# Performance work log

Measured on AMD Instinct MI355X. Metric: run time of the kernel, lower is better.

## Reference

```python
import jax, jax.numpy as jnp
import numpy as np

EPS = 1.1920929e-07  # torch fp32 RMSNorm default eps

def rmsnorm(x, w):
    return x * jax.lax.rsqrt(jnp.mean(x * x, axis=-1, keepdims=True) + EPS) * w

def causal_conv1d(x, w, b):
    # x: [B, L, di], w: [di, dc] depthwise kernel, b: [di]
    di, dc = w.shape
    xt = jnp.swapaxes(x, 1, 2)                       # [B, di, L]
    xt = jnp.pad(xt, ((0, 0), (0, 0), (dc - 1, 0)))  # causal left pad
    out = jax.lax.conv_general_dilated(
        xt, w[:, None, :], window_strides=(1,), padding='VALID',
        feature_group_count=di, dimension_numbers=('NCH', 'OIH', 'NCH'))
    return jnp.swapaxes(out + b[None, :, None], 1, 2)  # [B, L, di]

def selective_scan(u, dt, Bm, Cm, A, Dp):
    # u, dt: [B, L, di]; Bm, Cm: [B, L, ds]; A: [di, ds]; Dp: [di]
    Bsz, L, di = u.shape
    ds = A.shape[1]
    def step(h, inp):
        dt_t, B_t, C_t, u_t = inp
        dA = jnp.exp(dt_t[..., None] * A)                           # [B, di, ds]
        dBu = dt_t[..., None] * B_t[:, None, :] * u_t[..., None]    # [B, di, ds]
        h = dA * h + dBu
        y = jnp.einsum('bds,bs->bd', h, C_t)
        return h, y
    h0 = jnp.zeros((Bsz, di, ds), u.dtype)
    xs = (jnp.swapaxes(dt, 0, 1), jnp.swapaxes(Bm, 0, 1),
          jnp.swapaxes(Cm, 0, 1), jnp.swapaxes(u, 0, 1))
    _, ys = jax.lax.scan(step, h0, xs)                # ys: [L, B, di]
    return jnp.swapaxes(ys, 0, 1) + u * Dp            # skip connection D*u

def mamba_block(x, in_w, cw, cb, xp_w, dtp_w, dtp_b, a_log, dp, out_w, d_state, dt_rank):
    di = a_log.shape[0]
    xz = jnp.einsum('bld,ed->ble', x, in_w)           # [B, L, 2*di]
    x_in, z = xz[..., :di], xz[..., di:]
    xc = jax.nn.silu(causal_conv1d(x_in, cw, cb))     # [B, L, di]
    x_dbl = jnp.einsum('bld,ed->ble', xc, xp_w)       # [B, L, dt_rank+2*ds]
    dt = x_dbl[..., :dt_rank]
    Bm = x_dbl[..., dt_rank:dt_rank + d_state]
    Cm = x_dbl[..., dt_rank + d_state:]
    dt = jax.nn.softplus(jnp.einsum('blr,dr->bld', dt, dtp_w) + dtp_b)
    A = -jnp.exp(a_log)                               # [di, ds]
    y = selective_scan(xc, dt, Bm, Cm, A, dp)
    y = y * jax.nn.silu(z)
    return jnp.einsum('bld,ed->ble', y, out_w)        # [B, L, d_model]

def mlp(x, w1, b1, w2, b2):
    h = jax.nn.gelu(jnp.einsum('bld,ed->ble', x, w1) + b1, approximate=False)
    return jax.nn.gelu(jnp.einsum('ble,de->bld', h, w2) + b2, approximate=False)

def reference(x, in_proj_w, conv_w, conv_b, x_proj_w, dt_proj_w, dt_proj_b,
              A_log, D_param, out_proj_w, mlp_w1, mlp_b1, mlp_w2, mlp_b2,
              ln_w, ln2_w):
    d_state = A_log.shape[-1]
    dt_rank = dt_proj_w.shape[-1]
    num_layers = in_proj_w.shape[0]
    residual2 = x
    for i in range(num_layers):
        residual = x
        x = mamba_block(x, in_proj_w[i], conv_w[i], conv_b[i], x_proj_w[i],
                        dt_proj_w[i], dt_proj_b[i], A_log[i], D_param[i],
                        out_proj_w[i], d_state, dt_rank)
        x = mlp(x, mlp_w1, mlp_b1, mlp_w2, mlp_b2)
        x = rmsnorm(x + residual, ln_w)
    return rmsnorm(x + residual2, ln2_w)

def setup_inputs() -> dict:
    key = jax.random.key(0)
    ks = jax.random.split(key, 16)
    B, L, D = 4, 2048, 1024
    NL, di, ds, dc, dtr = 2, 2048, 16, 4, 64
    s = 0.02
    return {
        'x': jax.random.normal(ks[0], (B, L, D), jnp.float32),
        'in_proj_w': jax.random.normal(ks[1], (NL, 2 * di, D), jnp.float32) * s,
        'conv_w': jax.random.normal(ks[2], (NL, di, dc), jnp.float32) * 0.3,
        'conv_b': jax.random.normal(ks[3], (NL, di), jnp.float32) * 0.02,
        'x_proj_w': jax.random.normal(ks[4], (NL, dtr + 2 * ds, di), jnp.float32) * s,
        'dt_proj_w': jax.random.normal(ks[5], (NL, di, dtr), jnp.float32) * 0.1,
        'dt_proj_b': jax.random.normal(ks[6], (NL, di), jnp.float32) * 0.5 - 4.0,
        'A_log': jnp.log(jax.random.uniform(ks[7], (NL, di, ds), jnp.float32, 1.0, 16.0)),
        'D_param': jax.random.normal(ks[8], (NL, di), jnp.float32),
        'out_proj_w': jax.random.normal(ks[9], (NL, D, di), jnp.float32) * s,
        'mlp_w1': jax.random.normal(ks[10], (2 * D, D), jnp.float32) * s,
        'mlp_b1': jnp.zeros((2 * D,), jnp.float32),
        'mlp_w2': jax.random.normal(ks[11], (D, 2 * D), jnp.float32) * s,
        'mlp_b2': jnp.zeros((D,), jnp.float32),
        'ln_w': jnp.ones((D,), jnp.float32),
        'ln2_w': jnp.ones((D,), jnp.float32),
    }
```

## Files before the change

### kernel.cpp

```cpp
#include <hip/hip_runtime.h>
#include <math.h>

namespace {

constexpr int Bsz = 4;
constexpr int L   = 2048;
constexpr int D   = 1024;
constexpr int DI  = 2048;
constexpr int DSTATE = 16;
constexpr int DTR = 64;
constexpr int ML  = Bsz * L;
constexpr int NCH = 32;
constexpr int CL  = 64;

typedef __attribute__((ext_vector_type(8))) short bfrag;
typedef __attribute__((ext_vector_type(4))) float f32x4;

__device__ __forceinline__ unsigned short f2b(float f) {
  union { float f; unsigned int u; } c; c.f = f;
  unsigned int u = c.u;
  unsigned int r = (u + 0x7fffu + ((u >> 16) & 1u)) >> 16;
  return (unsigned short)r;
}
__device__ __forceinline__ float b2f(unsigned short h) {
  union { unsigned int u; float f; } c; c.u = ((unsigned int)h) << 16;
  return c.f;
}

__device__ __forceinline__ void async16(const void* g, void* l) {
  __builtin_amdgcn_global_load_lds(
      (const __attribute__((address_space(1))) void*)g,
      (__attribute__((address_space(3))) void*)l, 16, 0, 0);
}

template<int ACT>
__device__ __forceinline__ float activate(float x) {
  if (ACT == 1) { return x / (1.f + expf(-x)); }
  if (ACT == 2) { return 0.5f * x * (1.f + erff(x * 0.7071067811865475f)); }
  if (ACT == 3) { return (x > 20.f) ? x : log1pf(expf(x)); }
  return x;
}

template<int ACT, bool HAS_BIAS, int BN, bool SPLIT>
__global__ __launch_bounds__(512) void gemm2(
    const unsigned short* __restrict__ A, long lda,
    const unsigned short* __restrict__ W, long ldw,
    const float* __restrict__ bias,
    unsigned short* __restrict__ C0,
    unsigned short* __restrict__ C1,
    long ldc, int K)
{
  constexpr int NB   = BN / 64;
  constexpr int ABUF = 256 * 64;
  constexpr int BBUF = BN * 64;
  constexpr int NLA  = 4;
  constexpr int NLB  = NB;
  constexpr int NL   = NLA + NLB;
  __shared__ unsigned short lds[2 * ABUF + 2 * BBUF];

  const int tid  = threadIdx.x;
  const int lane = tid & 63;
  const int wid  = tid >> 6;
  const int wr   = wid >> 2;
  const int wc   = wid & 3;
  const int frow = lane & 15;
  const int klg  = lane >> 4;

  const int gx = gridDim.x;
  int id = blockIdx.y * gx + blockIdx.x;
  const int q = (gx * gridDim.y) >> 3;
  id = (id & 7) * q + (id >> 3);
  const int bx = id % gx;
  const int by = id / gx;
  const long bm = (long)by * 256;
  const long bn = (long)bx * BN;

  unsigned short* Cb;
  long cbase;
  if (SPLIT) {
    if (bn < 2048) { Cb = C0; cbase = bn; }
    else           { Cb = C1; cbase = bn - 2048; }
  } else { Cb = C0; cbase = bn; }

  f32x4 acc[8][NB];
  #pragma unroll
  for (int m = 0; m < 8; ++m)
    #pragma unroll
    for (int n = 0; n < NB; ++n)
      acc[m][n] = (f32x4){0.f, 0.f, 0.f, 0.f};

  auto stage = [&](int kt, int p) {
    const long kcol = (long)kt * 64;
    #pragma unroll
    for (int l = 0; l < NLA; ++l) {
      const int idx = tid + l * 512;
      const int row = idx >> 3;
      const int ch  = (idx & 7) ^ (row & 7);
      async16(A + (bm + row) * lda + kcol + ch * 8,
              &lds[p * ABUF + idx * 8]);
    }
    #pragma unroll
    for (int l = 0; l < NLB; ++l) {
      const int idx = tid + l * 512;
      const int row = idx >> 3;
      const int ch  = (idx & 7) ^ (row & 7);
      async16(W + (bn + row) * ldw + kcol + ch * 8,
              &lds[2 * ABUF + p * BBUF + idx * 8]);
    }
  };

  const int NT = K >> 6;
  stage(0, 0);
  stage(1, 1);
  asm volatile("s_waitcnt vmcnt(%0)" :: "n"(NL) : "memory");
  __builtin_amdgcn_sched_barrier(0);
  __builtin_amdgcn_s_barrier();

  for (int kt = 0; kt < NT; ++kt) {
    const unsigned short* Ab = &lds[(kt & 1) * ABUF];
    const unsigned short* Bb = &lds[2 * ABUF + (kt & 1) * BBUF];
    __builtin_amdgcn_s_setprio(1);
    #pragma unroll
    for (int kk = 0; kk < 2; ++kk) {
      bfrag av[8], bv[NB];
      #pragma unroll
      for (int m = 0; m < 8; ++m) {
        const int r  = wr * 128 + m * 16 + frow;
        const int ch = (kk * 4 + klg) ^ (r & 7);
        av[m] = *reinterpret_cast<const bfrag*>(&Ab[r * 64 + ch * 8]);
      }
      #pragma unroll
      for (int n = 0; n < NB; ++n) {
        const int r  = wc * (BN / 4) + n * 16 + frow;
        const int ch = (kk * 4 + klg) ^ (r & 7);
        bv[n] = *reinterpret_cast<const bfrag*>(&Bb[r * 64 + ch * 8]);
      }
      #pragma unroll
      for (int m = 0; m < 8; ++m)
        #pragma unroll
        for (int n = 0; n < NB; ++n)
          acc[m][n] = __builtin_amdgcn_mfma_f32_16x16x32_bf16(bv[n], av[m], acc[m][n], 0, 0, 0);
    }
    __builtin_amdgcn_s_setprio(0);
    if (kt + 1 == NT) break;
    __builtin_amdgcn_sched_barrier(0);
    __builtin_amdgcn_s_barrier();
    if (kt + 2 < NT) {
      stage(kt + 2, kt & 1);
      asm volatile("s_waitcnt vmcnt(%0)" :: "n"(NL) : "memory");
    } else {
      asm volatile("s_waitcnt vmcnt(0)" ::: "memory");
    }
    __builtin_amdgcn_sched_barrier(0);
    __builtin_amdgcn_s_barrier();
  }

  #pragma unroll
  for (int n = 0; n < NB; ++n) {
    const long coff = wc * (BN / 4) + n * 16 + klg * 4;
    float4 b4 = make_float4(0.f, 0.f, 0.f, 0.f);
    if (HAS_BIAS) b4 = *reinterpret_cast<const float4*>(&bias[bn + coff]);
    #pragma unroll
    for (int m = 0; m < 8; ++m) {
      const long row = bm + wr * 128 + m * 16 + frow;
      const float v0 = activate<ACT>(acc[m][n][0] + b4.x);
      const float v1 = activate<ACT>(acc[m][n][1] + b4.y);
      const float v2 = activate<ACT>(acc[m][n][2] + b4.z);
      const float v3 = activate<ACT>(acc[m][n][3] + b4.w);
      ushort4 o; o.x = f2b(v0); o.y = f2b(v1); o.z = f2b(v2); o.w = f2b(v3);
      *reinterpret_cast<ushort4*>(&Cb[row * ldc + cbase + coff]) = o;
    }
  }
}

template<int ACT, bool HAS_BIAS>
__global__ __launch_bounds__(256) void gemm_mfma(
    const unsigned short* __restrict__ A, long lda,
    const unsigned short* __restrict__ W, long ldw,
    const float* __restrict__ bias,
    unsigned short* __restrict__ C, long ldc,
    int K)
{
  __shared__ unsigned short As[128 * 32];
  __shared__ unsigned short Bs[128 * 32];
  const int tid  = threadIdx.x;
  const int lane = tid & 63;
  const int w    = tid >> 6;
  const int wr   = w >> 1, wc = w & 1;
  const long bm = (long)blockIdx.y * 128;
  const long bn = (long)blockIdx.x * 128;

  const int srow = tid >> 2;
  const int scol = (tid & 3) * 8;
  const unsigned short* ga0 = A + (bm + srow)      * lda + scol;
  const unsigned short* ga1 = A + (bm + 64 + srow) * lda + scol;
  const unsigned short* gb0 = W + (bn + srow)      * ldw + scol;
  const unsigned short* gb1 = W + (bn + 64 + srow) * ldw + scol;
  char* lA = (char*)As;
  char* lB = (char*)Bs;
  const int loff = tid * 16;

  const int frow = lane & 15;
  const int klg  = lane >> 4;
  const int fko  = klg * 8;

  f32x4 acc[4][4];
  #pragma unroll
  for (int m = 0; m < 4; ++m)
    #pragma unroll
    for (int n = 0; n < 4; ++n)
      acc[m][n] = (f32x4){0.f, 0.f, 0.f, 0.f};

  for (int k0 = 0; k0 < K; k0 += 32) {
    __syncthreads();
    async16(ga0 + k0, lA + loff);
    async16(ga1 + k0, lA + 4096 + loff);
    async16(gb0 + k0, lB + loff);
    async16(gb1 + k0, lB + 4096 + loff);
    __syncthreads();
    bfrag a[4], b[4];
    #pragma unroll
    for (int m = 0; m < 4; ++m)
      a[m] = *reinterpret_cast<const bfrag*>(&As[(wr*64 + m*16 + frow)*32 + fko]);
    #pragma unroll
    for (int n = 0; n < 4; ++n)
      b[n] = *reinterpret_cast<const bfrag*>(&Bs[(wc*64 + n*16 + frow)*32 + fko]);
    #pragma unroll
    for (int m = 0; m < 4; ++m)
      #pragma unroll
      for (int n = 0; n < 4; ++n)
        acc[m][n] = __builtin_amdgcn_mfma_f32_16x16x32_bf16(b[n], a[m], acc[m][n], 0, 0, 0);
  }

  #pragma unroll
  for (int n = 0; n < 4; ++n) {
    const long col = bn + wc*64 + n*16 + klg*4;
    float4 b4 = make_float4(0.f, 0.f, 0.f, 0.f);
    if (HAS_BIAS) b4 = *reinterpret_cast<const float4*>(&bias[col]);
    #pragma unroll
    for (int m = 0; m < 4; ++m) {
      const long row = bm + wr*64 + m*16 + frow;
      const float v0 = activate<ACT>(acc[m][n][0] + b4.x);
      const float v1 = activate<ACT>(acc[m][n][1] + b4.y);
      const float v2 = activate<ACT>(acc[m][n][2] + b4.z);
      const float v3 = activate<ACT>(acc[m][n][3] + b4.w);
      ushort4 o; o.x = f2b(v0); o.y = f2b(v1); o.z = f2b(v2); o.w = f2b(v3);
      *reinterpret_cast<ushort4*>(&C[row * ldc + col]) = o;
    }
  }
}

__global__ __launch_bounds__(256) void xproj_mfma(
    const unsigned short* __restrict__ A,
    const unsigned short* __restrict__ W,
    float* __restrict__ xdbl,
    unsigned short* __restrict__ dtr)
{
  constexpr int ABUF = 64 * 64;
  constexpr int BBUF = 96 * 64;
  constexpr int NL   = 5;
  __shared__ unsigned short lds[2 * ABUF + 2 * BBUF];

  const int tid  = threadIdx.x;
  const int lane = tid & 63;
  const int wv   = tid >> 6;
  const int frow = lane & 15;
  const int klg  = lane >> 4;
  const long bm  = (long)blockIdx.x * 64;

  f32x4 acc[6];
  #pragma unroll
  for (int n = 0; n < 6; ++n) acc[n] = (f32x4){0.f, 0.f, 0.f, 0.f};

  auto stage = [&](int kt, int p) {
    const long kcol = (long)kt * 64;
    #pragma unroll
    for (int l = 0; l < 2; ++l) {
      const int idx = tid + l * 256;
      const int row = idx >> 3;
      const int ch  = (idx & 7) ^ (row & 7);
      async16(A + (bm + row) * DI + kcol + ch * 8,
              &lds[p * ABUF + idx * 8]);
    }
    #pragma unroll
    for (int l = 0; l < 3; ++l) {
      const int idx = tid + l * 256;
      const int row = idx >> 3;
      const int ch  = (idx & 7) ^ (row & 7);
      async16(W + (long)row * DI + kcol + ch * 8,
              &lds[2 * ABUF + p * BBUF + idx * 8]);
    }
  };

  constexpr int NT = DI / 64;
  stage(0, 0);
  stage(1, 1);
  asm volatile("s_waitcnt vmcnt(%0)" :: "n"(NL) : "memory");
  __builtin_amdgcn_sched_barrier(0);
  __builtin_amdgcn_s_barrier();

  for (int kt = 0; kt < NT; ++kt) {
    const unsigned short* Ab = &lds[(kt & 1) * ABUF];
    const unsigned short* Bb = &lds[2 * ABUF + (kt & 1) * BBUF];
    __builtin_amdgcn_s_setprio(1);
    #pragma unroll
    for (int kk = 0; kk < 2; ++kk) {
      const int ra = wv * 16 + frow;
      const int cha = (kk * 4 + klg) ^ (ra & 7);
      const bfrag a = *reinterpret_cast<const bfrag*>(&Ab[ra * 64 + cha * 8]);
      #pragma unroll
      for (int n = 0; n < 6; ++n) {
        const int rb = n * 16 + frow;
        const int chb = (kk * 4 + klg) ^ (rb & 7);
        const bfrag b = *reinterpret_cast<const bfrag*>(&Bb[rb * 64 + chb * 8]);
        acc[n] = __builtin_amdgcn_mfma_f32_16x16x32_bf16(b, a, acc[n], 0, 0, 0);
      }
    }
    __builtin_amdgcn_s_setprio(0);
    if (kt + 1 == NT) break;
    __builtin_amdgcn_sched_barrier(0);
    __builtin_amdgcn_s_barrier();
    if (kt + 2 < NT) {
      stage(kt + 2, kt & 1);
      asm volatile("s_waitcnt vmcnt(%0)" :: "n"(NL) : "memory");
    } else {
      asm volatile("s_waitcnt vmcnt(0)" ::: "memory");
    }
    __builtin_amdgcn_sched_barrier(0);
    __builtin_amdgcn_s_barrier();
  }

  const long row = bm + wv*16 + frow;
  #pragma unroll
  for (int n = 0; n < 6; ++n) {
    const int col = n*16 + klg*4;
    float4 v; v.x = acc[n][0]; v.y = acc[n][1]; v.z = acc[n][2]; v.w = acc[n][3];
    *reinterpret_cast<float4*>(&xdbl[row * 96 + col]) = v;
    if (n < 4) {
      ushort4 o; o.x = f2b(v.x); o.y = f2b(v.y); o.z = f2b(v.z); o.w = f2b(v.w);
      *reinterpret_cast<ushort4*>(&dtr[row * 64 + col]) = o;
    }
  }
}

__global__ __launch_bounds__(256) void cvt_all(
    const float* __restrict__ s0, unsigned short* __restrict__ d0, long n0,
    const float* __restrict__ s1, unsigned short* __restrict__ d1, long n1,
    const float* __restrict__ s2, unsigned short* __restrict__ d2, long n2,
    const float* __restrict__ s3, unsigned short* __restrict__ d3, long n3,
    const float* __restrict__ s4, unsigned short* __restrict__ d4, long n4,
    const float* __restrict__ s5, unsigned short* __restrict__ d5, long n5,
    const float* __restrict__ s6, unsigned short* __restrict__ d6, long n6)
{
  long i = (long)blockIdx.x * 256 + threadIdx.x;
  const float* s; unsigned short* d;
  if      (i < n0)                    { s = s0; d = d0; }
  else if ((i -= n0) < n1)            { s = s1; d = d1; }
  else if ((i -= n1) < n2)            { s = s2; d = d2; }
  else if ((i -= n2) < n3)            { s = s3; d = d3; }
  else if ((i -= n3) < n4)            { s = s4; d = d4; }
  else if ((i -= n4) < n5)            { s = s5; d = d5; }
  else if ((i -= n5) < n6)            { s = s6; d = d6; }
  else return;
  const float4 v = reinterpret_cast<const float4*>(s)[i];
  ushort4 o; o.x = f2b(v.x); o.y = f2b(v.y); o.z = f2b(v.z); o.w = f2b(v.w);
  reinterpret_cast<ushort4*>(d)[i] = o;
}

__global__ __launch_bounds__(256) void conv_silu(
    const unsigned short* __restrict__ xin,
    const float* __restrict__ w,
    const float* __restrict__ bias,
    unsigned short* __restrict__ xc)
{
  const int idx = blockIdx.x * 256 + threadIdx.x;
  const int D4 = DI / 4;
  const int d  = (idx % D4) * 4;
  const int bt = idx / D4;
  const int t  = bt & (L - 1);
  const int b  = bt >> 11;
  const float4 w0 = *reinterpret_cast<const float4*>(w + (long)(d+0)*4);
  const float4 w1 = *reinterpret_cast<const float4*>(w + (long)(d+1)*4);
  const float4 w2 = *reinterpret_cast<const float4*>(w + (long)(d+2)*4);
  const float4 w3 = *reinterpret_cast<const float4*>(w + (long)(d+3)*4);
  const float4 bv = *reinterpret_cast<const float4*>(bias + d);
  float a0 = bv.x, a1 = bv.y, a2 = bv.z, a3 = bv.w;
  const float wk0[4] = {w0.x, w0.y, w0.z, w0.w};
  const float wk1[4] = {w1.x, w1.y, w1.z, w1.w};
  const float wk2[4] = {w2.x, w2.y, w2.z, w2.w};
  const float wk3[4] = {w3.x, w3.y, w3.z, w3.w};
  #pragma unroll
  for (int k = 0; k < 4; ++k) {
    const int tt = t - 3 + k;
    if (tt >= 0) {
      const ushort4 xv = *reinterpret_cast<const ushort4*>(xin + ((long)(b * L + tt)) * DI + d);
      a0 = fmaf(wk0[k], b2f(xv.x), a0);
      a1 = fmaf(wk1[k], b2f(xv.y), a1);
      a2 = fmaf(wk2[k], b2f(xv.z), a2);
      a3 = fmaf(wk3[k], b2f(xv.w), a3);
    }
  }
  a0 = a0 / (1.f + expf(-a0));
  a1 = a1 / (1.f + expf(-a1));
  a2 = a2 / (1.f + expf(-a2));
  a3 = a3 / (1.f + expf(-a3));
  ushort4 o; o.x = f2b(a0); o.y = f2b(a1); o.z = f2b(a2); o.w = f2b(a3);
  *reinterpret_cast<ushort4*>(xc + (long)bt * DI + d) = o;
}

__global__ __launch_bounds__(256) void scan_p1(
    const unsigned short* __restrict__ dt,
    const unsigned short* __restrict__ u,
    const float* __restrict__ xdbl,
    const float* __restrict__ a_log,
    float* __restrict__ hend,
    float* __restrict__ sdt)
{
  const int bid = blockIdx.x;
  const int dg = bid & 7;
  const int c  = (bid >> 3) & (NCH - 1);
  const int b  = bid >> 8;
  const int d  = dg * 256 + threadIdx.x;
  float A[16];
  #pragma unroll
  for (int q = 0; q < 4; ++q) {
    const float4 al = *reinterpret_cast<const float4*>(a_log + (long)d * 16 + q * 4);
    A[q*4+0] = -__expf(al.x); A[q*4+1] = -__expf(al.y);
    A[q*4+2] = -__expf(al.z); A[q*4+3] = -__expf(al.w);
  }
  float h[16];
  #pragma unroll
  for (int s = 0; s < 16; ++s) h[s] = 0.f;
  float s_dt = 0.f;
  const long row0 = (long)b * L + (long)c * CL;

  float dtv = b2f(dt[row0 * DI + d]);
  float uv  = b2f(u [row0 * DI + d]);
  float4 Bq[4];
  #pragma unroll
  for (int q = 0; q < 4; ++q)
    Bq[q] = *reinterpret_cast<const float4*>(xdbl + row0 * 96 + 64 + q * 4);

  for (int t = 0; t < CL; ++t) {
    float dtn = 0.f, un = 0.f;
    float4 Bn[4] = {};
    if (t + 1 < CL) {
      const long r2 = row0 + t + 1;
      dtn = b2f(dt[r2 * DI + d]);
      un  = b2f(u [r2 * DI + d]);
      #pragma unroll
      for (int q = 0; q < 4; ++q)
        Bn[q] = *reinterpret_cast<const float4*>(xdbl + r2 * 96 + 64 + q * 4);
    }
    const float Bv[16] = {Bq[0].x,Bq[0].y,Bq[0].z,Bq[0].w, Bq[1].x,Bq[1].y,Bq[1].z,Bq[1].w,
                          Bq[2].x,Bq[2].y,Bq[2].z,Bq[2].w, Bq[3].x,Bq[3].y,Bq[3].z,Bq[3].w};
    s_dt += dtv;
    const float dtu = dtv * uv;
    #pragma unroll
    for (int s = 0; s < 16; ++s)
      h[s] = fmaf(__expf(dtv * A[s]), h[s], dtu * Bv[s]);
    dtv = dtn; uv = un;
    #pragma unroll
    for (int q = 0; q < 4; ++q) Bq[q] = Bn[q];
  }
  const long cb = (long)(b * NCH + c);
  #pragma unroll
  for (int s = 0; s < 16; ++s)
    hend[(cb * 16 + s) * DI + d] = h[s];
  sdt[cb * DI + d] = s_dt;
}

__global__ __launch_bounds__(256) void scan_p2(
    float* __restrict__ hend,
    const float* __restrict__ sdt,
    const float* __restrict__ a_log)
{
  const long idx = (long)blockIdx.x * 256 + threadIdx.x;
  const int d = idx & (DI - 1);
  const int s = (idx >> 11) & 15;
  const int b = idx >> 15;
  const float A = -__expf(a_log[(long)d * 16 + s]);
  float h = 0.f;
  for (int c = 0; c < NCH; ++c) {
    const long cb = (long)(b * NCH + c);
    const long off = (cb * 16 + s) * DI + d;
    const float hl = hend[off];
    const float sd = sdt[cb * DI + d];
    hend[off] = h;
    h = fmaf(__expf(A * sd), h, hl);
  }
}

__global__ __launch_bounds__(256) void scan_p3(
    const unsigned short* __restrict__ dt,
    const unsigned short* __restrict__ u,
    const float* __restrict__ xdbl,
    const unsigned short* __restrict__ z,
    const float* __restrict__ a_log,
    const float* __restrict__ dpar,
    const float* __restrict__ hinit,
    unsigned short* __restrict__ y)
{
  const int bid = blockIdx.x;
  const int dg = bid & 7;
  const int c  = (bid >> 3) & (NCH - 1);
  const int b  = bid >> 8;
  const int d  = dg * 256 + threadIdx.x;
  float A[16];
  #pragma unroll
  for (int q = 0; q < 4; ++q) {
    const float4 al = *reinterpret_cast<const float4*>(a_log + (long)d * 16 + q * 4);
    A[q*4+0] = -__expf(al.x); A[q*4+1] = -__expf(al.y);
    A[q*4+2] = -__expf(al.z); A[q*4+3] = -__expf(al.w);
  }
  const float Dv = dpar[d];
  const long cb = (long)(b * NCH + c);
  float h[16];
  #pragma unroll
  for (int s = 0; s < 16; ++s)
    h[s] = hinit[(cb * 16 + s) * DI + d];
  const long row0 = (long)b * L + (long)c * CL;

  float dtv = b2f(dt[row0 * DI + d]);
  float uv  = b2f(u [row0 * DI + d]);
  float zv  = b2f(z [row0 * DI + d]);
  float4 BCq[8];
  #pragma unroll
  for (int q = 0; q < 8; ++q)
    BCq[q] = *reinterpret_cast<const float4*>(xdbl + row0 * 96 + 64 + q * 4);

  for (int t = 0; t < CL; ++t) {
    float dtn = 0.f, un = 0.f, zn = 0.f;
    float4 BCn[8] = {};
    if (t + 1 < CL) {
      const long r2 = row0 + t + 1;
      dtn = b2f(dt[r2 * DI + d]);
      un  = b2f(u [r2 * DI + d]);
      zn  = b2f(z [r2 * DI + d]);
      #pragma unroll
      for (int q = 0; q < 8; ++q)
        BCn[q] = *reinterpret_cast<const float4*>(xdbl + r2 * 96 + 64 + q * 4);
    }
    const float Bv[16] = {BCq[0].x,BCq[0].y,BCq[0].z,BCq[0].w, BCq[1].x,BCq[1].y,BCq[1].z,BCq[1].w,
                          BCq[2].x,BCq[2].y,BCq[2].z,BCq[2].w, BCq[3].x,BCq[3].y,BCq[3].z,BCq[3].w};
    const float Cv[16] = {BCq[4].x,BCq[4].y,BCq[4].z,BCq[4].w, BCq[5].x,BCq[5].y,BCq[5].z,BCq[5].w,
                          BCq[6].x,BCq[6].y,BCq[6].z,BCq[6].w, BCq[7].x,BCq[7].y,BCq[7].z,BCq[7].w};
    const float dtu = dtv * uv;
    float yv = 0.f;
    #pragma unroll
    for (int s = 0; s < 16; ++s) {
      h[s] = fmaf(__expf(dtv * A[s]), h[s], dtu * Bv[s]);
      yv = fmaf(h[s], Cv[s], yv);
    }
    const float sg = zv / (1.f + __expf(-zv));
    y[(row0 + t) * DI + d] = f2b(fmaf(uv, Dv, yv) * sg);
    dtv = dtn; uv = un; zv = zn;
    #pragma unroll
    for (int q = 0; q < 8; ++q) BCq[q] = BCn[q];
  }
}

template<bool BIN, bool WBF>
__global__ __launch_bounds__(256) void add_rmsnorm(
    const void* __restrict__ xinp, const float* __restrict__ res,
    const float* __restrict__ w, float* __restrict__ out,
    unsigned short* __restrict__ xb)
{
  const int row = blockIdx.x;
  const int tid = threadIdx.x;
  const long base = (long)row * D;
  float4 v;
  if (BIN) {
    const ushort4 t = *reinterpret_cast<const ushort4*>((const unsigned short*)xinp + base + tid * 4);
    v.x = b2f(t.x); v.y = b2f(t.y); v.z = b2f(t.z); v.w = b2f(t.w);
  } else {
    v = *reinterpret_cast<const float4*>((const float*)xinp + base + tid * 4);
  }
  const float4 r = *reinterpret_cast<const float4*>(res + base + tid * 4);
  v.x += r.x; v.y += r.y; v.z += r.z; v.w += r.w;
  float ss = v.x*v.x + v.y*v.y + v.z*v.z + v.w*v.w;
  #pragma unroll
  for (int m = 1; m < 64; m <<= 1) ss += __shfl_xor(ss, m);
  __shared__ float red[4];
  if ((tid & 63) == 0) red[tid >> 6] = ss;
  __syncthreads();
  const float tot = red[0] + red[1] + red[2] + red[3];
  const float scale = rsqrtf(tot * (1.f / (float)D) + 1.1920929e-07f);
  const float4 wv = *reinterpret_cast<const float4*>(w + tid * 4);
  float4 o;
  o.x = v.x * scale * wv.x;
  o.y = v.y * scale * wv.y;
  o.z = v.z * scale * wv.z;
  o.w = v.w * scale * wv.w;
  *reinterpret_cast<float4*>(out + base + tid * 4) = o;
  if (WBF) {
    ushort4 ob; ob.x = f2b(o.x); ob.y = f2b(o.y); ob.z = f2b(o.z); ob.w = f2b(o.w);
    *reinterpret_cast<ushort4*>(xb + base + tid * 4) = ob;
  }
}

}

extern "C" void kernel_launch(void* const* d_in, const int* in_sizes, int n_in,
                              void* d_out, int out_size, void* d_ws, size_t ws_size,
                              hipStream_t stream)
{
  const float* x0     = (const float*)d_in[0];
  const float* in_w   = (const float*)d_in[1];
  const float* conv_w = (const float*)d_in[2];
  const float* conv_b = (const float*)d_in[3];
  const float* xp_w   = (const float*)d_in[4];
  const float* dtp_w  = (const float*)d_in[5];
  const float* dtp_b  = (const float*)d_in[6];
  const float* a_log  = (const float*)d_in[7];
  const float* d_par  = (const float*)d_in[8];
  const float* out_w  = (const float*)d_in[9];
  const float* w1     = (const float*)d_in[10];
  const float* b1     = (const float*)d_in[11];
  const float* w2     = (const float*)d_in[12];
  const float* b2     = (const float*)d_in[13];
  const float* ln_w   = (const float*)d_in[14];
  const float* ln2_w  = (const float*)d_in[15];
  float* out = (float*)d_out;

  char* ws = (char*)d_ws;
  unsigned short* in_wb  = (unsigned short*)(ws);
  unsigned short* out_wb = (unsigned short*)(ws + (16UL  << 20));
  unsigned short* w1b    = (unsigned short*)(ws + (24UL  << 20));
  unsigned short* w2b    = (unsigned short*)(ws + (28UL  << 20));
  unsigned short* xbf    = (unsigned short*)(ws + (32UL  << 20));
  unsigned short* zb     = (unsigned short*)(ws + (48UL  << 20));
  unsigned short* xc     = (unsigned short*)(ws + (80UL  << 20));
  float*          xdbl   = (float*)(ws + (112UL << 20));
  float*          sdtb   = (float*)(ws + (115UL << 20));
  float*          hendb  = (float*)(ws + (116UL << 20));
  unsigned short* xinb   = (unsigned short*)(ws + (132UL << 20));
  unsigned short* dtb    = xinb;
  unsigned short* ybf    = (unsigned short*)(ws + (164UL << 20));
  unsigned short* hm     = ybf;
  unsigned short* mo     = (unsigned short*)(ws + (196UL << 20));
  unsigned short* t2     = mo;
  unsigned short* xp_wb  = (unsigned short*)(ws + (212UL << 20));
  unsigned short* dtp_wb = (unsigned short*)(ws + (213UL << 20));
  unsigned short* dtrb   = (unsigned short*)(ws + (214UL << 20));

  const dim3 blk(256);
  const dim3 blk5(512);

  {
    const long n0 = 2L*2*DI*D/4, n1 = 2L*D*DI/4, n2 = 2L*D*D/4, n3 = 2L*D*D/4;
    const long n4 = 2L*96*DI/4,  n5 = 2L*DI*DTR/4, n6 = (long)ML*D/4;
    const long tot = n0+n1+n2+n3+n4+n5+n6;
    cvt_all<<<dim3((tot + 255)/256), blk, 0, stream>>>(
        in_w, in_wb, n0,  out_w, out_wb, n1,  w1, w1b, n2,  w2, w2b, n3,
        xp_w, xp_wb, n4,  dtp_w, dtp_wb, n5,  x0, xbf, n6);
  }

  const float* xcur = x0;
  for (int layer = 0; layer < 2; ++layer) {
    const long lo = (long)layer;
    const unsigned short* Winb = in_wb + lo * 2 * DI * D;
    gemm2<0,false,256,true><<<dim3(16, 32), blk5, 0, stream>>>(
        xbf, D, Winb, D, nullptr, xinb, zb, DI, D);
    conv_silu<<<dim3((long)ML*DI/4/256), blk, 0, stream>>>(
        xinb, conv_w + lo*DI*4, conv_b + lo*DI, xc);
    xproj_mfma<<<dim3(ML/64), blk, 0, stream>>>(
        xc, xp_wb + lo*96*DI, xdbl, dtrb);
    gemm_mfma<3,true><<<dim3(DI/128, ML/128), blk, 0, stream>>>(
        dtrb, DTR, dtp_wb + lo*DI*DTR, DTR, dtp_b + lo*DI, dtb, DI, DTR);
    scan_p1<<<dim3(Bsz*NCH*(DI/256)), blk, 0, stream>>>(
        dtb, xc, xdbl, a_log + lo*DI*DSTATE, hendb, sdtb);
    scan_p2<<<dim3(Bsz*DSTATE*DI/256), blk, 0, stream>>>(
        hendb, sdtb, a_log + lo*DI*DSTATE);
    scan_p3<<<dim3(Bsz*NCH*(DI/256)), blk, 0, stream>>>(
        dtb, xc, xdbl, zb, a_log + lo*DI*DSTATE, d_par + lo*DI, hendb, ybf);
    gemm2<0,false,128,false><<<dim3(8, 32), blk5, 0, stream>>>(
        ybf, DI, out_wb + lo*D*DI, DI, nullptr, mo, nullptr, D, DI);
    gemm2<2,true,256,false><<<dim3(8, 32), blk5, 0, stream>>>(
        mo, D, w1b, D, b1, hm, nullptr, 2*D, D);
    gemm2<2,true,128,false><<<dim3(8, 32), blk5, 0, stream>>>(
        hm, 2*D, w2b, 2*D, b2, t2, nullptr, D, 2*D);
    add_rmsnorm<true,true><<<dim3(ML), blk, 0, stream>>>(t2, xcur, ln_w, out, xbf);
    xcur = out;
  }
  add_rmsnorm<false,false><<<dim3(ML), blk, 0, stream>>>(out, x0, ln2_w, out, nullptr);
}
```

Before: 1.080 ms.

## Interleave async tile loads with MFMA phases in GEMM main loop

Restructures the bf16 GEMM main loop into four half-tile compute phases per K step, issuing the next tile's B and A-half loads between phases instead of in one bulk stage after the compute. A is split by row halves so each half's LDS buffer can be refilled as soon as its MFMAs finish. The goal is to hide global-to-LDS latency and cut the idle time at barriers, at the cost of more barriers per K step and tighter vmcnt accounting that could be fragile.

```diff
diff --git a/kernel.cpp b/kernel.cpp
--- a/kernel.cpp
+++ b/kernel.cpp
@@ -42,7 +42,7 @@
 }
 
 template<int ACT, bool HAS_BIAS, int BN, bool SPLIT>
-__global__ __launch_bounds__(512) void gemm2(
+__global__ __launch_bounds__(512) void gemm4(
     const unsigned short* __restrict__ A, long lda,
     const unsigned short* __restrict__ W, long ldw,
     const float* __restrict__ bias,
@@ -53,9 +53,7 @@
   constexpr int NB   = BN / 64;
   constexpr int ABUF = 256 * 64;
   constexpr int BBUF = BN * 64;
-  constexpr int NLA  = 4;
-  constexpr int NLB  = NB;
-  constexpr int NL   = NLA + NLB;
+  constexpr int UB   = NB;
   __shared__ unsigned short lds[2 * ABUF + 2 * BBUF];
 
   const int tid  = threadIdx.x;
@@ -89,70 +87,86 @@
     for (int n = 0; n < NB; ++n)
       acc[m][n] = (f32x4){0.f, 0.f, 0.f, 0.f};
 
-  auto stage = [&](int kt, int p) {
+  auto stageB = [&](int kt) {
     const long kcol = (long)kt * 64;
-    #pragma unroll
-    for (int l = 0; l < NLA; ++l) {
+    unsigned short* dst = &lds[2 * ABUF + (kt & 1) * BBUF];
+    #pragma unroll
+    for (int l = 0; l < UB; ++l) {
       const int idx = tid + l * 512;
       const int row = idx >> 3;
       const int ch  = (idx & 7) ^ (row & 7);
-      async16(A + (bm + row) * lda + kcol + ch * 8,
-              &lds[p * ABUF + idx * 8]);
-    }
-    #pragma unroll
-    for (int l = 0; l < NLB; ++l) {
+      async16(W + (bn + row) * ldw + kcol + ch * 8, dst + idx * 8);
+    }
+  };
+  auto stageA = [&](int kt, int mh) {
+    const long kcol = (long)kt * 64;
+    unsigned short* dst = &lds[(kt & 1) * ABUF];
+    #pragma unroll
+    for (int l = 0; l < 2; ++l) {
       const int idx = tid + l * 512;
-      const int row = idx >> 3;
+      const int rl  = idx >> 3;
+      const int row = mh * 64 + (rl & 63) + (rl >> 6) * 128;
       const int ch  = (idx & 7) ^ (row & 7);
-      async16(W + (bn + row) * ldw + kcol + ch * 8,
-              &lds[2 * ABUF + p * BBUF + idx * 8]);
+      async16(A + (bm + row) * lda + kcol + ch * 8, dst + row * 64 + (idx & 7) * 8);
     }
   };
 
   const int NT = K >> 6;
-  stage(0, 0);
-  stage(1, 1);
-  asm volatile("s_waitcnt vmcnt(%0)" :: "n"(NL) : "memory");
+  stageB(0); stageA(0, 0); stageA(0, 1);
+  asm volatile("s_waitcnt vmcnt(%0)" :: "n"(2) : "memory");
   __builtin_amdgcn_sched_barrier(0);
   __builtin_amdgcn_s_barrier();
 
   for (int kt = 0; kt < NT; ++kt) {
     const unsigned short* Ab = &lds[(kt & 1) * ABUF];
     const unsigned short* Bb = &lds[2 * ABUF + (kt & 1) * BBUF];
-    __builtin_amdgcn_s_setprio(1);
+    const bool pf = (kt + 1 < NT);
     #pragma unroll
     for (int kk = 0; kk < 2; ++kk) {
-      bfrag av[8], bv[NB];
-      #pragma unroll
-      for (int m = 0; m < 8; ++m) {
-        const int r  = wr * 128 + m * 16 + frow;
-        const int ch = (kk * 4 + klg) ^ (r & 7);
-        av[m] = *reinterpret_cast<const bfrag*>(&Ab[r * 64 + ch * 8]);
+      bfrag bv[NB], av[4];
+      #pragma unroll
+      for (int n = 0; n < NB; ++n) {
+        const int r = wc * (BN / 4) + n * 16 + frow;
+        bv[n] = *reinterpret_cast<const bfrag*>(&Bb[r * 64 + ((kk * 4 + klg) ^ (r & 7)) * 8]);
       }
       #pragma unroll
-      for (int n = 0; n < NB; ++n) {
-        const int r  = wc * (BN / 4) + n * 16 + frow;
-        const int ch = (kk * 4 + klg) ^ (r & 7);
-        bv[n] = *reinterpret_cast<const bfrag*>(&Bb[r * 64 + ch * 8]);
+      for (int m = 0; m < 4; ++m) {
+        const int r = wr * 128 + m * 16 + frow;
+        av[m] = *reinterpret_cast<const bfrag*>(&Ab[r * 64 + ((kk * 4 + klg) ^ (r & 7)) * 8]);
       }
-      #pragma unroll
-      for (int m = 0; m < 8; ++m)
+      if (pf) { if (kk == 0) stageB(kt + 1); else stageA(kt + 1, 1); }
+      __builtin_amdgcn_s_setprio(1);
+      #pragma unroll
+      for (int m = 0; m < 4; ++m)
         #pragma unroll
         for (int n = 0; n < NB; ++n)
           acc[m][n] = __builtin_amdgcn_mfma_f32_16x16x32_bf16(bv[n], av[m], acc[m][n], 0, 0, 0);
-    }
-    __builtin_amdgcn_s_setprio(0);
-    if (kt + 1 == NT) break;
-    __builtin_amdgcn_sched_barrier(0);
-    __builtin_amdgcn_s_barrier();
-    if (kt + 2 < NT) {
-      stage(kt + 2, kt & 1);
-      asm volatile("s_waitcnt vmcnt(%0)" :: "n"(NL) : "memory");
-    } else {
-      asm volatile("s_waitcnt vmcnt(0)" ::: "memory");
-    }
-    __builtin_amdgcn_sched_barrier(0);
-    __builtin_amdgcn_s_barrier();
+      __builtin_amdgcn_s_setprio(0);
+      if (kk == 0) {
+        asm volatile("s_waitcnt vmcnt(%0)" :: "n"(UB) : "memory");
+      }
+      __builtin_amdgcn_sched_barrier(0);
+      __builtin_amdgcn_s_barrier();
+      #pragma unroll
+      for (int m = 0; m < 4; ++m) {
+        const int r = wr * 128 + 64 + m * 16 + frow;
+        av[m] = *reinterpret_cast<const bfrag*>(&Ab[r * 64 + ((kk * 4 + klg) ^ (r & 7)) * 8]);
+      }
+      if (pf && kk == 0) stageA(kt + 1, 0);
+      __builtin_amdgcn_s_setprio(1);
+      #pragma unroll
+      for (int m = 0; m < 4; ++m)
+        #pragma unroll
+        for (int n = 0; n < NB; ++n)
+          acc[4 + m][n] = __builtin_amdgcn_mfma_f32_16x16x32_bf16(bv[n], av[m], acc[4 + m][n], 0, 0, 0);
+      __builtin_amdgcn_s_setprio(0);
+      if (kk == 1) {
+        if (kt + 1 == NT) break;
+        asm volatile("s_waitcnt vmcnt(%0)" :: "n"(2) : "memory");
+      }
+      __builtin_amdgcn_sched_barrier(0);
+      __builtin_amdgcn_s_barrier();
+    }
   }
 
   #pragma unroll
@@ -660,7 +674,7 @@
   for (int layer = 0; layer < 2; ++layer) {
     const long lo = (long)layer;
     const unsigned short* Winb = in_wb + lo * 2 * DI * D;
-    gemm2<0,false,256,true><<<dim3(16, 32), blk5, 0, stream>>>(
+    gemm4<0,false,256,true><<<dim3(16, 32), blk5, 0, stream>>>(
         xbf, D, Winb, D, nullptr, xinb, zb, DI, D);
     conv_silu<<<dim3((long)ML*DI/4/256), blk, 0, stream>>>(
         xinb, conv_w + lo*DI*4, conv_b + lo*DI, xc);
@@ -674,11 +688,11 @@
         hendb, sdtb, a_log + lo*DI*DSTATE);
     scan_p3<<<dim3(Bsz*NCH*(DI/256)), blk, 0, stream>>>(
         dtb, xc, xdbl, zb, a_log + lo*DI*DSTATE, d_par + lo*DI, hendb, ybf);
-    gemm2<0,false,128,false><<<dim3(8, 32), blk5, 0, stream>>>(
+    gemm4<0,false,128,false><<<dim3(8, 32), blk5, 0, stream>>>(
         ybf, DI, out_wb + lo*D*DI, DI, nullptr, mo, nullptr, D, DI);
-    gemm2<2,true,256,false><<<dim3(8, 32), blk5, 0, stream>>>(
+    gemm4<2,true,256,false><<<dim3(8, 32), blk5, 0, stream>>>(
         mo, D, w1b, D, b1, hm, nullptr, 2*D, D);
-    gemm2<2,true,128,false><<<dim3(8, 32), blk5, 0, stream>>>(
+    gemm4<2,true,128,false><<<dim3(8, 32), blk5, 0, stream>>>(
         hm, 2*D, w2b, 2*D, b2, t2, nullptr, D, 2*D);
     add_rmsnorm<true,true><<<dim3(ML), blk, 0, stream>>>(t2, xcur, ln_w, out, xbf);
     xcur = out;
```

Measured after the change: 1.104 ms. 1.02x slower.
